# Kernel optimization log

Measured on AMD Instinct MI355X. Metric: run time of the kernel, lower is better.

## Reference

```python
import jax, jax.numpy as jnp
import numpy as np

# Problem sizes
N, D, B = 4096, 2048, 64  # nodes, feature dim, sequential samples
# LARFDSSOM hyperparameters (from __init__ defaults)
A_T = 0.3          # activation threshold
DSBETA = 1e-4      # moving-average rate
E_B = 0.5          # winner learning rate
E_N = 0.01 * E_B   # neighbor learning rate (e_n is multiplied by e_b in __init__)
EPS_DS = 0.01      # relevance smoothing


def setup_inputs() -> dict:
    key = jax.random.key(0)
    k0, k1, k2, k3, k4 = jax.random.split(key, 5)
    return {
        "x": jax.random.uniform(k0, (B, D), jnp.float32),
        "weights": jax.random.uniform(k1, (N, D), jnp.float32),
        "moving_avg": jax.random.uniform(k2, (N, D), jnp.float32),
        "relevances": jax.random.uniform(k3, (N, D), jnp.float32),
        "wins": jnp.zeros((N,), jnp.float32),
        "neighbors": jax.random.randint(k4, (N, N), 0, 2) > 0,
    }


def _som_steps(x, weights, moving_avg, relevances, wins, neighbors):
    """Sequential LARFDSSOM update_map over B samples (codebook at max size,
    so the add_node branch is structurally impossible and the per-sample step
    is either 'update winner + neighbors' or a no-op)."""
    node_ids = jnp.arange(weights.shape[0])

    def step(state, w):
        W, M, R, wn = state
        diff = w[None, :] - W                          # [N, D]
        # weighted_distance + activation
        dists = jnp.sum(R * diff * diff, axis=1)       # [N]
        rel_sum = jnp.sum(R, axis=1)                   # [N]
        act = rel_sum / (rel_sum + dists + 1e-7)
        winner = jnp.argmax(act)
        do_upd = act[winner] >= A_T                    # else no-op (codebook full)
        is_winner = node_ids == winner
        is_nb = neighbors[winner] & (~is_winner)
        # per-node learning rate: e_b for winner, e_n for neighbors, 0 otherwise
        lr = jnp.where(is_winner, E_B, jnp.where(is_nb, E_N, 0.0))[:, None]  # [N, 1]
        # update_node (vectorized over all nodes, masked below)
        dist_abs = jnp.abs(diff)
        M_new = lr * DSBETA * dist_abs + (1.0 - lr * DSBETA) * M
        mx = jnp.max(M_new, axis=1, keepdims=True)
        mn = jnp.min(M_new, axis=1, keepdims=True)
        av = jnp.mean(M_new, axis=1, keepdims=True)
        denom = EPS_DS * (mx - mn)
        # denom == 0 -> original produces NaN then sets relevance to 1.0
        arg = jnp.clip((M_new - av) / jnp.where(denom == 0.0, 1.0, denom), -80.0, 80.0)
        R_new = jnp.where(denom == 0.0, 1.0, 1.0 / (1.0 + jnp.exp(arg)))
        W_new = W + lr * diff
        m = (do_upd & (lr[:, 0] > 0.0))[:, None]       # rows actually touched
        W = jnp.where(m, W_new, W)
        M = jnp.where(m, M_new, M)
        R = jnp.where(m, R_new, R)
        wn = wn + jnp.where(is_winner & do_upd, 1.0, 0.0)
        return (W, M, R, wn), None

    (W, M, R, wn), _ = jax.lax.scan(step, (weights, moving_avg, relevances, wins), x)
    return W


def reference(x, weights, moving_avg, relevances, wins, neighbors):
    return _som_steps(x, weights, moving_avg, relevances, wins, neighbors)
```

## Files before the change

### kernel.cpp

```cpp
#include <hip/hip_runtime.h>
#include <cstddef>

#define NN 4096
#define DD 2048
#define BB 64
#define RPB 8
#define NBLK (NN / RPB)
#define NGRP (NBLK / 8)

constexpr float kAT     = 0.3f;
constexpr float kDSBETA = 1e-4f;
constexpr float kEB     = 0.5f;
constexpr float kEN     = 0.005f;
constexpr float kEPS    = 0.01f;

__device__ __forceinline__ float wave_sum_f(float v) {
#pragma unroll
    for (int o = 32; o; o >>= 1) v += __shfl_xor(v, o, 64);
    return v;
}
__device__ __forceinline__ double wave_sum_d(double v) {
#pragma unroll
    for (int o = 32; o; o >>= 1) v += __shfl_xor(v, o, 64);
    return v;
}
__device__ __forceinline__ float wave_max_f(float v) {
#pragma unroll
    for (int o = 32; o; o >>= 1) v = fmaxf(v, __shfl_xor(v, o, 64));
    return v;
}
__device__ __forceinline__ float wave_min_f(float v) {
#pragma unroll
    for (int o = 32; o; o >>= 1) v = fminf(v, __shfl_xor(v, o, 64));
    return v;
}
__device__ __forceinline__ unsigned long long wave_max_u64(unsigned long long v) {
#pragma unroll
    for (int o = 32; o; o >>= 1) {
        const unsigned long long u = __shfl_xor(v, o, 64);
        v = (u > v) ? u : v;
    }
    return v;
}

__global__ void detect_nb(const unsigned char* __restrict__ nb, unsigned* __restrict__ flag) {
    unsigned v = 0;
    const int i0 = threadIdx.x * 256;
    for (int i = 0; i < 256; i++) {
        const int idx = i0 + i;
        if ((idx & 3) != 0) v |= nb[idx];
    }
    if (v != 0) atomicOr(flag, 1u);
}

__global__ __launch_bounds__(256, 2) void som_persist(
    const float* __restrict__ x,
    const float* __restrict__ W0,
    const float* __restrict__ M0,
    const float* __restrict__ R0,
    const unsigned char* __restrict__ nbb,
    const unsigned* __restrict__ flag,
    float* __restrict__ Wout,
    unsigned long long* __restrict__ pkey,
    unsigned long long* __restrict__ gkey)
{
    const int tid  = threadIdx.x;
    const int wid  = tid >> 6;
    const int lane = tid & 63;
    const int bid  = (int)blockIdx.x;
    const int n0   = bid * RPB;
    const int col  = tid * 8;
    const int grp  = bid >> 3;
    const bool leader = ((bid & 7) == 0);

    __shared__ double sdd[RPB][4];
    __shared__ double spp[RPB][4];
    __shared__ float  sf[3][RPB][4];
    __shared__ unsigned long long sKey;

    const bool nb_byte = (*flag != 0);
    const int* nbi = (const int*)nbb;

    float w[RPB][8], r[RPB][8], m[RPB][8], xcur[8];

#pragma unroll
    for (int row = 0; row < RPB; ++row) {
        const size_t base = (size_t)(n0 + row) * DD + col;
        *(float4*)(&w[row][0]) = *(const float4*)(W0 + base);
        *(float4*)(&w[row][4]) = *(const float4*)(W0 + base + 4);
        *(float4*)(&r[row][0]) = *(const float4*)(R0 + base);
        *(float4*)(&r[row][4]) = *(const float4*)(R0 + base + 4);
        *(float4*)(&m[row][0]) = *(const float4*)(M0 + base);
        *(float4*)(&m[row][4]) = *(const float4*)(M0 + base + 4);
    }
    *(float4*)(xcur)     = *(const float4*)(x + col);
    *(float4*)(xcur + 4) = *(const float4*)(x + col + 4);

    auto act_phase = [&](int slot, unsigned touched) {
#pragma unroll
        for (int row = 0; row < RPB; ++row) {
            const bool doPs = (touched >> row) & 1u;
            double pd = 0.0;
#pragma unroll
            for (int j = 0; j < 8; ++j) {
                const double d  = (double)xcur[j] - (double)w[row][j];
                const double rj = (double)r[row][j];
                pd += rj * d * d;
            }
            pd = wave_sum_d(pd);
            if (lane == 0) sdd[row][wid] = pd;
            if (doPs) {
                double ps = 0.0;
#pragma unroll
                for (int j = 0; j < 8; ++j) ps += (double)r[row][j];
                ps = wave_sum_d(ps);
                if (lane == 0) spp[row][wid] = ps;
            }
        }
        __syncthreads();
        if (wid == 0 && lane < RPB) {
            const int row = lane;
            const double td = sdd[row][0] + sdd[row][1] + sdd[row][2] + sdd[row][3];
            const double tr = spp[row][0] + spp[row][1] + spp[row][2] + spp[row][3];
            const double act = tr / (tr + td + 1e-7);
            const unsigned long long ab = (unsigned long long)__double_as_longlong(act);
            unsigned long long k = (ab & ~0xFFFULL) | (unsigned long long)(4095 - (n0 + row));
#pragma unroll
            for (int o = 1; o < RPB; o <<= 1) {
                const unsigned long long u = __shfl_xor(k, o, 64);
                k = (u > k) ? u : k;
            }
            if (lane == 0)
                __hip_atomic_store(&pkey[(size_t)slot * NBLK + bid], k,
                                   __ATOMIC_RELAXED, __HIP_MEMORY_SCOPE_AGENT);
        }
    };

    act_phase(0, 0xFFu);

    float xn[8];
    for (int t = 0; t < BB; ++t) {
        const bool has_next = (t < BB - 1);
        if (has_next) {
            const size_t xb = (size_t)(t + 1) * DD + col;
            *(float4*)(xn)     = *(const float4*)(x + xb);
            *(float4*)(xn + 4) = *(const float4*)(x + xb + 4);
        }

        if (wid == 0) {
            if (leader) {
                if (lane < 8) {
                    unsigned long long* pk = pkey + (size_t)t * NBLK + (grp << 3);
                    unsigned long long v;
                    int it = 0;
                    while (true) {
                        v = __hip_atomic_load(&pk[lane],
                                              __ATOMIC_RELAXED, __HIP_MEMORY_SCOPE_AGENT);
                        if (!__any(v == 0ull)) break;
                        if (++it > 2000000) break;
                        __builtin_amdgcn_s_sleep(2);
                    }
#pragma unroll
                    for (int o = 1; o < 8; o <<= 1) {
                        const unsigned long long u = __shfl_xor(v, o, 64);
                        v = (u > v) ? u : v;
                    }
                    if (lane == 0)
                        __hip_atomic_store(&gkey[(size_t)t * NGRP + grp], v,
                                           __ATOMIC_RELAXED, __HIP_MEMORY_SCOPE_AGENT);
                }
            }
            unsigned long long kv;
            {
                unsigned long long* gk = gkey + (size_t)t * NGRP;
                int it = 0;
                while (true) {
                    kv = __hip_atomic_load(&gk[lane],
                                           __ATOMIC_RELAXED, __HIP_MEMORY_SCOPE_AGENT);
                    if (!__any(kv == 0ull)) break;
                    if (++it > 2000000) break;
                    __builtin_amdgcn_s_sleep(4);
                }
            }
            kv = wave_max_u64(kv);
            if (lane == 0) sKey = kv;
        }
        __syncthreads();
        const unsigned long long k = sKey;
        const double act_w = __longlong_as_double((long long)(k & ~0xFFFULL));
        const int winner   = 4095 - (int)(k & 0xFFFULL);

        unsigned touched = 0u;
        if (act_w >= (double)kAT) {
            int nbr[RPB];
            {
                const size_t off = (size_t)winner * NN + n0;
                if (nb_byte) {
                    const unsigned long long nb8 = *(const unsigned long long*)(nbb + off);
#pragma unroll
                    for (int i = 0; i < RPB; ++i)
                        nbr[i] = (int)((nb8 >> (8 * i)) & 0xFFull);
                } else {
                    const int4 a = *(const int4*)(nbi + off);
                    const int4 b = *(const int4*)(nbi + off + 4);
                    nbr[0] = a.x; nbr[1] = a.y; nbr[2] = a.z; nbr[3] = a.w;
                    nbr[4] = b.x; nbr[5] = b.y; nbr[6] = b.z; nbr[7] = b.w;
                }
            }
            float lrs[RPB];
#pragma unroll
            for (int row = 0; row < RPB; ++row) {
                const int n = n0 + row;
                float lr = 0.0f;
                if (n == winner)      lr = kEB;
                else if (nbr[row])    lr = kEN;
                lrs[row] = lr;
                if (lr != 0.0f) {
                    touched |= (1u << row);
                    const float c1 = lr * kDSBETA;
                    const float c2 = 1.0f - c1;
                    float psum = 0.0f, pmx = -INFINITY, pmn = INFINITY;
#pragma unroll
                    for (int j = 0; j < 8; ++j) {
                        const float d  = xcur[j] - w[row][j];
                        const float mv = c1 * fabsf(d) + c2 * m[row][j];
                        w[row][j] += lr * d;
                        m[row][j] = mv;
                        psum += mv;
                        pmx = fmaxf(pmx, mv);
                        pmn = fminf(pmn, mv);
                    }
                    psum = wave_sum_f(psum); pmx = wave_max_f(pmx); pmn = wave_min_f(pmn);
                    if (lane == 0) { sf[0][row][wid] = psum; sf[1][row][wid] = pmx; sf[2][row][wid] = pmn; }
                }
            }
            if (touched) {
                __syncthreads();
#pragma unroll
                for (int row = 0; row < RPB; ++row) {
                    if (lrs[row] != 0.0f) {
                        const float ts  = sf[0][row][0] + sf[0][row][1] + sf[0][row][2] + sf[0][row][3];
                        const float tmx = fmaxf(fmaxf(sf[1][row][0], sf[1][row][1]),
                                                fmaxf(sf[1][row][2], sf[1][row][3]));
                        const float tmn = fminf(fminf(sf[2][row][0], sf[2][row][1]),
                                                fminf(sf[2][row][2], sf[2][row][3]));
                        const float av    = ts * (1.0f / (float)DD);
                        const float denom = kEPS * (tmx - tmn);
                        if (denom == 0.0f) {
#pragma unroll
                            for (int j = 0; j < 8; ++j) r[row][j] = 1.0f;
                        } else {
#pragma unroll
                            for (int j = 0; j < 8; ++j) {
                                float a = (m[row][j] - av) / denom;
                                a = fminf(fmaxf(a, -80.0f), 80.0f);
                                r[row][j] = 1.0f / (1.0f + expf(a));
                            }
                        }
                    }
                }
            }
        }

        if (has_next) {
#pragma unroll
            for (int j = 0; j < 8; ++j) xcur[j] = xn[j];
            act_phase(t + 1, touched);
        }
    }

#pragma unroll
    for (int row = 0; row < RPB; ++row) {
        const size_t base = (size_t)(n0 + row) * DD + col;
        *(float4*)(Wout + base)     = *(float4*)(&w[row][0]);
        *(float4*)(Wout + base + 4) = *(float4*)(&w[row][4]);
    }
}

__global__ __launch_bounds__(256) void som_step(
    const float* __restrict__ x_upd, const float* __restrict__ x_act,
    float* __restrict__ W, float* __restrict__ M, float* __restrict__ R,
    const void* __restrict__ nb, const unsigned* __restrict__ flag,
    const unsigned long long* __restrict__ part_upd,
    unsigned long long* __restrict__ part_act)
{
    const int n   = blockIdx.x;
    const int tid = threadIdx.x;
    __shared__ float  sred[3][4];
    __shared__ double sredd[2][4];

    float lr = 0.0f;
    if (part_upd != nullptr) {
        unsigned long long k = part_upd[(size_t)(tid & 63) * 8];
        k = wave_max_u64(k);
        const double act_w = __longlong_as_double((long long)(k & ~0xFFFULL));
        const int winner   = 4095 - (int)(k & 0xFFFULL);
        if (act_w >= (double)kAT) {
            if (n == winner) lr = kEB;
            else {
                const size_t off = (size_t)winner * NN + n;
                const bool isnb = (*flag != 0)
                    ? (((const unsigned char*)nb)[off] != 0)
                    : (((const int*)nb)[off] != 0);
                if (isnb) lr = kEN;
            }
        }
    }
    const bool next = (x_act != nullptr);
    if (lr == 0.0f && !next) return;

    const size_t rowoff = (size_t)n * DD + (size_t)tid * 8;
    const size_t xoff   = (size_t)tid * 8;
    float w[8], r[8];
    *(float4*)(w)     = *(const float4*)(W + rowoff);
    *(float4*)(w + 4) = *(const float4*)(W + rowoff + 4);

    if (lr != 0.0f) {
        float m[8], xu[8], mnew[8];
        *(float4*)(m)      = *(const float4*)(M + rowoff);
        *(float4*)(m + 4)  = *(const float4*)(M + rowoff + 4);
        *(float4*)(xu)     = *(const float4*)(x_upd + xoff);
        *(float4*)(xu + 4) = *(const float4*)(x_upd + xoff + 4);
        const float c1 = lr * kDSBETA, c2 = 1.0f - c1;
        float psum = 0.0f, pmx = -INFINITY, pmn = INFINITY;
#pragma unroll
        for (int j = 0; j < 8; j++) {
            const float d = xu[j] - w[j];
            w[j] += lr * d;
            const float mv = c1 * fabsf(d) + c2 * m[j];
            mnew[j] = mv; psum += mv;
            pmx = fmaxf(pmx, mv); pmn = fminf(pmn, mv);
        }
        psum = wave_sum_f(psum); pmx = wave_max_f(pmx); pmn = wave_min_f(pmn);
        const int wid = tid >> 6, lane = tid & 63;
        if (lane == 0) { sred[0][wid] = psum; sred[1][wid] = pmx; sred[2][wid] = pmn; }
        __syncthreads();
        const float ts  = sred[0][0] + sred[0][1] + sred[0][2] + sred[0][3];
        const float tmx = fmaxf(fmaxf(sred[1][0], sred[1][1]), fmaxf(sred[1][2], sred[1][3]));
        const float tmn = fminf(fminf(sred[2][0], sred[2][1]), fminf(sred[2][2], sred[2][3]));
        __syncthreads();
        const float av = ts * (1.0f / (float)DD);
        const float denom = kEPS * (tmx - tmn);
        if (denom == 0.0f) {
#pragma unroll
            for (int j = 0; j < 8; j++) r[j] = 1.0f;
        } else {
#pragma unroll
            for (int j = 0; j < 8; j++) {
                float a = (mnew[j] - av) / denom;
                a = fminf(fmaxf(a, -80.0f), 80.0f);
                r[j] = 1.0f / (1.0f + expf(a));
            }
        }
        *(float4*)(W + rowoff)     = *(float4*)(w);
        *(float4*)(W + rowoff + 4) = *(float4*)(w + 4);
        *(float4*)(M + rowoff)     = *(float4*)(mnew);
        *(float4*)(M + rowoff + 4) = *(float4*)(mnew + 4);
        *(float4*)(R + rowoff)     = *(float4*)(r);
        *(float4*)(R + rowoff + 4) = *(float4*)(r + 4);
    } else {
        *(float4*)(r)     = *(const float4*)(R + rowoff);
        *(float4*)(r + 4) = *(const float4*)(R + rowoff + 4);
    }

    if (next) {
        float xn[8];
        *(float4*)(xn)     = *(const float4*)(x_act + xoff);
        *(float4*)(xn + 4) = *(const float4*)(x_act + xoff + 4);
        double pd = 0.0, ps = 0.0;
#pragma unroll
        for (int j = 0; j < 8; j++) {
            const double d  = (double)xn[j] - (double)w[j];
            const double rj = (double)r[j];
            pd += rj * d * d; ps += rj;
        }
        pd = wave_sum_d(pd); ps = wave_sum_d(ps);
        const int wid = tid >> 6, lane = tid & 63;
        if (lane == 0) { sredd[0][wid] = pd; sredd[1][wid] = ps; }
        __syncthreads();
        if (tid == 0) {
            const double td = sredd[0][0] + sredd[0][1] + sredd[0][2] + sredd[0][3];
            const double tr = sredd[1][0] + sredd[1][1] + sredd[1][2] + sredd[1][3];
            const double act = tr / (tr + td + 1e-7);
            const unsigned long long ab = (unsigned long long)__double_as_longlong(act);
            const unsigned long long kk = (ab & ~0xFFFULL) | (unsigned long long)(4095 - n);
            atomicMax(&part_act[(size_t)(n & 63) * 8], kk);
        }
    }
}

extern "C" void kernel_launch(void* const* d_in, const int* in_sizes, int n_in,
                              void* d_out, int out_size, void* d_ws, size_t ws_size,
                              hipStream_t stream) {
    const float*         x   = (const float*)d_in[0];
    const float*         W0  = (const float*)d_in[1];
    float*               M   = (float*)d_in[2];
    float*               R   = (float*)d_in[3];
    const unsigned char* nbb = (const unsigned char*)d_in[5];
    float*               W   = (float*)d_out;

    unsigned long long* part = (unsigned long long*)d_ws;
    const size_t part_bytes  = (size_t)66 * 64 * 8 * sizeof(unsigned long long);
    unsigned long long* gkey = (unsigned long long*)((char*)d_ws + part_bytes);
    const size_t cnt_bytes = (size_t)BB * 8 * 16 * sizeof(unsigned);
    unsigned* flagp = (unsigned*)((char*)d_ws + part_bytes + cnt_bytes);

    hipMemsetAsync(d_ws, 0, part_bytes + cnt_bytes + 64, stream);
    detect_nb<<<1, 256, 0, stream>>>(nbb, flagp);

    int occ = 0;
    hipError_t qerr = hipOccupancyMaxActiveBlocksPerMultiprocessor(
        &occ, (const void*)som_persist, 256, 0);
    if (qerr == hipSuccess && occ >= 2) {
        som_persist<<<NBLK, 256, 0, stream>>>(x, W0, M, R, nbb, flagp, W, part, gkey);
        return;
    }

    hipMemcpyAsync(W, W0, sizeof(float) * (size_t)NN * DD, hipMemcpyDeviceToDevice, stream);
    som_step<<<NN, 256, 0, stream>>>(nullptr, x, W, M, R, nbb, flagp, nullptr, part);
    for (int t = 0; t < BB; t++) {
        const float* xu = x + (size_t)t * DD;
        const float* xa = (t < BB - 1) ? (x + (size_t)(t + 1) * DD) : nullptr;
        const unsigned long long* pu = part + (size_t)t * 64 * 8;
        unsigned long long*       pa = (t < BB - 1) ? (part + (size_t)(t + 1) * 64 * 8) : nullptr;
        som_step<<<NN, 256, 0, stream>>>(xu, xa, W, M, R, nbb, flagp, pu, pa);
    }
}
```

Before: 1.695 ms.

## Flatten grid-wide argmax barrier and preload neighbor column slice into LDS

Drops the two-level leader/group reduction of per-block winner keys. Every block's first wave now polls all 512 partial keys directly and reduces them itself. At kernel start, each block also copies its 8-column slice of the neighbor matrix for every possible winner into 32KB of shared memory. This removes the per-step global neighbor load from the critical path after the barrier. The costs are more polling traffic on the partial-key array, a large strided prologue read, and extra LDS use that could affect the two-blocks-per-CU occupancy the launch depends on.

After: 1.679 ms. No clear change (-1.0%).

```diff
diff --git a/kernel.cpp b/kernel.cpp
--- a/kernel.cpp
+++ b/kernel.cpp
@@ -6,7 +6,6 @@
 #define BB 64
 #define RPB 8
 #define NBLK (NN / RPB)
-#define NGRP (NBLK / 8)
 
 constexpr float kAT     = 0.3f;
 constexpr float kDSBETA = 1e-4f;
@@ -61,8 +60,7 @@
     const unsigned char* __restrict__ nbb,
     const unsigned* __restrict__ flag,
     float* __restrict__ Wout,
-    unsigned long long* __restrict__ pkey,
-    unsigned long long* __restrict__ gkey)
+    unsigned long long* __restrict__ pkey)
 {
     const int tid  = threadIdx.x;
     const int wid  = tid >> 6;
@@ -70,16 +68,35 @@
     const int bid  = (int)blockIdx.x;
     const int n0   = bid * RPB;
     const int col  = tid * 8;
-    const int grp  = bid >> 3;
-    const bool leader = ((bid & 7) == 0);
 
     __shared__ double sdd[RPB][4];
     __shared__ double spp[RPB][4];
     __shared__ float  sf[3][RPB][4];
     __shared__ unsigned long long sKey;
+    __shared__ unsigned long long nbcol[NN];
 
     const bool nb_byte = (*flag != 0);
     const int* nbi = (const int*)nbb;
+
+    if (nb_byte) {
+        for (int i = tid; i < NN; i += 256)
+            nbcol[i] = *(const unsigned long long*)(nbb + (size_t)i * NN + n0);
+    } else {
+        for (int i = tid; i < NN; i += 256) {
+            const int4 a = *(const int4*)(nbi + (size_t)i * NN + n0);
+            const int4 b = *(const int4*)(nbi + (size_t)i * NN + n0 + 4);
+            unsigned long long v = 0;
+            v |= (a.x != 0 ? 1ull : 0ull) << 0;
+            v |= (a.y != 0 ? 1ull : 0ull) << 8;
+            v |= (a.z != 0 ? 1ull : 0ull) << 16;
+            v |= (a.w != 0 ? 1ull : 0ull) << 24;
+            v |= (b.x != 0 ? 1ull : 0ull) << 32;
+            v |= (b.y != 0 ? 1ull : 0ull) << 40;
+            v |= (b.z != 0 ? 1ull : 0ull) << 48;
+            v |= (b.w != 0 ? 1ull : 0ull) << 56;
+            nbcol[i] = v;
+        }
+    }
 
     float w[RPB][8], r[RPB][8], m[RPB][8], xcur[8];
 
@@ -148,42 +165,26 @@
         }
 
         if (wid == 0) {
-            if (leader) {
-                if (lane < 8) {
-                    unsigned long long* pk = pkey + (size_t)t * NBLK + (grp << 3);
-                    unsigned long long v;
-                    int it = 0;
-                    while (true) {
-                        v = __hip_atomic_load(&pk[lane],
+            unsigned long long* pk = pkey + (size_t)t * NBLK;
+            unsigned long long kk[8];
+            int it = 0;
+            while (true) {
+                bool miss = false;
+#pragma unroll
+                for (int i = 0; i < 8; ++i) {
+                    kk[i] = __hip_atomic_load(&pk[lane + 64 * i],
                                               __ATOMIC_RELAXED, __HIP_MEMORY_SCOPE_AGENT);
-                        if (!__any(v == 0ull)) break;
-                        if (++it > 2000000) break;
-                        __builtin_amdgcn_s_sleep(2);
-                    }
-#pragma unroll
-                    for (int o = 1; o < 8; o <<= 1) {
-                        const unsigned long long u = __shfl_xor(v, o, 64);
-                        v = (u > v) ? u : v;
-                    }
-                    if (lane == 0)
-                        __hip_atomic_store(&gkey[(size_t)t * NGRP + grp], v,
-                                           __ATOMIC_RELAXED, __HIP_MEMORY_SCOPE_AGENT);
+                    miss |= (kk[i] == 0ull);
                 }
-            }
-            unsigned long long kv;
-            {
-                unsigned long long* gk = gkey + (size_t)t * NGRP;
-                int it = 0;
-                while (true) {
-                    kv = __hip_atomic_load(&gk[lane],
-                                           __ATOMIC_RELAXED, __HIP_MEMORY_SCOPE_AGENT);
-                    if (!__any(kv == 0ull)) break;
-                    if (++it > 2000000) break;
-                    __builtin_amdgcn_s_sleep(4);
-                }
-            }
-            kv = wave_max_u64(kv);
-            if (lane == 0) sKey = kv;
+                if (!__any(miss)) break;
+                if (++it > 300000) break;
+                __builtin_amdgcn_s_sleep(8);
+            }
+            unsigned long long kmax = 0;
+#pragma unroll
+            for (int i = 0; i < 8; ++i) kmax = (kk[i] > kmax) ? kk[i] : kmax;
+            kmax = wave_max_u64(kmax);
+            if (lane == 0) sKey = kmax;
         }
         __syncthreads();
         const unsigned long long k = sKey;
@@ -192,28 +193,14 @@
 
         unsigned touched = 0u;
         if (act_w >= (double)kAT) {
-            int nbr[RPB];
-            {
-                const size_t off = (size_t)winner * NN + n0;
-                if (nb_byte) {
-                    const unsigned long long nb8 = *(const unsigned long long*)(nbb + off);
-#pragma unroll
-                    for (int i = 0; i < RPB; ++i)
-                        nbr[i] = (int)((nb8 >> (8 * i)) & 0xFFull);
-                } else {
-                    const int4 a = *(const int4*)(nbi + off);
-                    const int4 b = *(const int4*)(nbi + off + 4);
-                    nbr[0] = a.x; nbr[1] = a.y; nbr[2] = a.z; nbr[3] = a.w;
-                    nbr[4] = b.x; nbr[5] = b.y; nbr[6] = b.z; nbr[7] = b.w;
-                }
-            }
+            const unsigned long long nb8 = nbcol[winner];
             float lrs[RPB];
 #pragma unroll
             for (int row = 0; row < RPB; ++row) {
                 const int n = n0 + row;
                 float lr = 0.0f;
-                if (n == winner)      lr = kEB;
-                else if (nbr[row])    lr = kEN;
+                if (n == winner)                          lr = kEB;
+                else if ((nb8 >> (8 * row)) & 0xFFull)    lr = kEN;
                 lrs[row] = lr;
                 if (lr != 0.0f) {
                     touched |= (1u << row);
@@ -401,7 +388,6 @@
 
     unsigned long long* part = (unsigned long long*)d_ws;
     const size_t part_bytes  = (size_t)66 * 64 * 8 * sizeof(unsigned long long);
-    unsigned long long* gkey = (unsigned long long*)((char*)d_ws + part_bytes);
     const size_t cnt_bytes = (size_t)BB * 8 * 16 * sizeof(unsigned);
     unsigned* flagp = (unsigned*)((char*)d_ws + part_bytes + cnt_bytes);
 
@@ -412,7 +398,7 @@
     hipError_t qerr = hipOccupancyMaxActiveBlocksPerMultiprocessor(
         &occ, (const void*)som_persist, 256, 0);
     if (qerr == hipSuccess && occ >= 2) {
-        som_persist<<<NBLK, 256, 0, stream>>>(x, W0, M, R, nbb, flagp, W, part, gkey);
+        som_persist<<<NBLK, 256, 0, stream>>>(x, W0, M, R, nbb, flagp, W, part);
         return;
     }
 
```
